# Optimization experiments

Measured on AMD Instinct MI355X. Metric: run time of the kernel, lower is better.

Reference implementation:

```python
import jax, jax.numpy as jnp
import numpy as np

THETA = 1.0
V_TH = 1.0       # spikingjelly IFNode default v_threshold
SG_ALPHA = 4.0   # spikingjelly surrogate.Sigmoid default alpha


@jax.custom_vjp
def heaviside(x):
    # spike = 1 if membrane - threshold >= 0
    return (x >= 0).astype(x.dtype)

def _heaviside_fwd(x):
    return (x >= 0).astype(x.dtype), x

def _heaviside_bwd(x, g):
    s = jax.nn.sigmoid(SG_ALPHA * x)
    return (g * SG_ALPHA * s * (1.0 - s),)

heaviside.defvjp(_heaviside_fwd, _heaviside_bwd)


@jax.custom_vjp
def spike_aggregate(spike_out, z_total):
    return spike_out

def _sa_fwd(spike_out, z_total):
    return spike_out, z_total

def _sa_bwd(z_total, g):
    surrogate = (z_total > 0).astype(g.dtype) / THETA
    return (jnp.zeros_like(g), g * surrogate)

spike_aggregate.defvjp(_sa_fwd, _sa_bwd)


def setup_inputs() -> dict:
    key = jax.random.key(0)
    k_x, k_w1, k_b1, k_w2, k_b2 = jax.random.split(key, 5)
    B, D_in, H, D_out = 4096, 784, 800, 10
    x = jax.random.uniform(k_x, (B, D_in), dtype=jnp.float32)
    # nn.Linear-style init: U(-1/sqrt(fan_in), 1/sqrt(fan_in))
    s1 = 1.0 / np.sqrt(D_in)
    s2 = 1.0 / np.sqrt(H)
    W1 = jax.random.uniform(k_w1, (H, D_in), jnp.float32, -s1, s1)
    b1 = jax.random.uniform(k_b1, (H,), jnp.float32, -s1, s1)
    W2 = jax.random.uniform(k_w2, (D_out, H), jnp.float32, -s2, s2)
    b2 = jax.random.uniform(k_b2, (D_out,), jnp.float32, -s2, s2)
    return {"x": x, "W1": W1, "b1": b1, "W2": W2, "b2": b2, "T_sim": 32}


def reference(x, W1, b1, W2, b2, T_sim):
    B = x.shape[0]
    x = x.reshape(B, -1)
    # fixed Bernoulli rate encoding (rand_like(x) < x)
    u = jax.random.uniform(jax.random.key(42), x.shape, dtype=x.dtype)
    x_fixed = (u < x).astype(x.dtype)
    # fc1 input is the same every timestep -> compute once
    cur1 = x_fixed @ W1.T + b1                     # [B, 800]

    def step(carry, _):
        v1, v2, count, z_total = carry
        h1 = v1 + cur1
        spk1 = heaviside(h1 - V_TH)
        v1 = h1 * (1.0 - jax.lax.stop_gradient(spk1))  # hard reset to 0, detach_reset
        cur2 = spk1 @ W2.T + b2                    # [B, 10]
        z_total = z_total + cur2
        h2 = v2 + cur2
        spk2 = heaviside(h2 - V_TH)
        v2 = h2 * (1.0 - jax.lax.stop_gradient(spk2))
        count = count + spk2
        return (v1, v2, count, z_total), None

    H, D_out = W1.shape[0], W2.shape[0]
    init = (jnp.zeros((B, H), x.dtype), jnp.zeros((B, D_out), x.dtype),
            jnp.zeros((B, D_out), x.dtype), jnp.zeros((B, D_out), x.dtype))
    (v1, v2, count, z_total), _ = jax.lax.scan(step, init, None, length=T_sim)
    return spike_aggregate(count, z_total)
```

## Files before the change

### kernel.cpp

```cpp
#include <hip/hip_runtime.h>
#include <stdint.h>

#define B_ROWS 4096
#define D_IN   784
#define H_DIM  800
#define D_OUT  10
#define T_SIM  32
#define N_ELEM (B_ROWS * D_IN)
#define CAP    448

__device__ __forceinline__ void threefry2x32(uint32_t k0, uint32_t k1,
                                             uint32_t& x0, uint32_t& x1) {
  uint32_t ks0 = k0, ks1 = k1, ks2 = k0 ^ k1 ^ 0x1BD11BDAu;
  x0 += ks0; x1 += ks1;
#define TF_RND(r) { x0 += x1; x1 = (x1 << (r)) | (x1 >> (32 - (r))); x1 ^= x0; }
  TF_RND(13) TF_RND(15) TF_RND(26) TF_RND(6)
  x0 += ks1; x1 += ks2 + 1u;
  TF_RND(17) TF_RND(29) TF_RND(16) TF_RND(24)
  x0 += ks2; x1 += ks0 + 2u;
  TF_RND(13) TF_RND(15) TF_RND(26) TF_RND(6)
  x0 += ks0; x1 += ks1 + 3u;
  TF_RND(17) TF_RND(29) TF_RND(16) TF_RND(24)
  x0 += ks1; x1 += ks2 + 4u;
  TF_RND(13) TF_RND(15) TF_RND(26) TF_RND(6)
  x0 += ks2; x1 += ks0 + 5u;
#undef TF_RND
}

__global__ __launch_bounds__(256) void gen_xfixed(const float* __restrict__ x,
                                                  float* __restrict__ xf) {
  int i = blockIdx.x * blockDim.x + threadIdx.x;
  if (i >= N_ELEM) return;
  uint32_t c0 = 0u, c1 = (uint32_t)i;
  threefry2x32(0u, 42u, c0, c1);
  uint32_t bits = c0 ^ c1;
  float u = __uint_as_float((bits >> 9) | 0x3F800000u) - 1.0f;
  xf[i] = (u < x[i]) ? 1.0f : 0.0f;
}

#define BM 128
#define BN 64
#define BK 16

__global__ __launch_bounds__(256) void gemm_masks(const float* __restrict__ xf,
                                                  const float* __restrict__ W1,
                                                  const float* __restrict__ b1,
                                                  uint32_t* __restrict__ mb) {
  __shared__ __align__(16) float As[BK][BM + 4];
  __shared__ __align__(16) float Bs[BK][BN + 4];
  const int m0 = blockIdx.y * BM;
  const int n0 = blockIdx.x * BN;
  const int t  = threadIdx.x;
  const int tx = t & 15;
  const int ty = t >> 4;
  const int sM = t >> 2;
  const int sK = (t & 3) * 4;
  const int hB = n0 + sM;
  const bool bOK = (hB < H_DIM);
  const float* aptr0 = xf + (size_t)(m0 + sM) * D_IN + sK;
  const float* aptr1 = xf + (size_t)(m0 + 64 + sM) * D_IN + sK;
  const float* bptr  = W1 + (size_t)(bOK ? hB : 0) * D_IN + sK;

  float4 a4a = *(const float4*)(aptr0);
  float4 a4b = *(const float4*)(aptr1);
  float4 b4  = *(const float4*)(bptr);
  if (!bOK) { b4.x = b4.y = b4.z = b4.w = 0.0f; }

  float acc[8][4] = {};
  for (int kt = 0; kt < D_IN; kt += BK) {
    As[sK + 0][sM] = a4a.x; As[sK + 1][sM] = a4a.y;
    As[sK + 2][sM] = a4a.z; As[sK + 3][sM] = a4a.w;
    As[sK + 0][64 + sM] = a4b.x; As[sK + 1][64 + sM] = a4b.y;
    As[sK + 2][64 + sM] = a4b.z; As[sK + 3][64 + sM] = a4b.w;
    Bs[sK + 0][sM] = b4.x; Bs[sK + 1][sM] = b4.y;
    Bs[sK + 2][sM] = b4.z; Bs[sK + 3][sM] = b4.w;
    __syncthreads();
    if (kt + BK < D_IN) {
      a4a = *(const float4*)(aptr0 + kt + BK);
      a4b = *(const float4*)(aptr1 + kt + BK);
      b4  = *(const float4*)(bptr + kt + BK);
      if (!bOK) { b4.x = b4.y = b4.z = b4.w = 0.0f; }
    }
#pragma unroll
    for (int kk = 0; kk < BK; kk++) {
      float4 av0 = *(const float4*)&As[kk][ty * 8];
      float4 av1 = *(const float4*)&As[kk][ty * 8 + 4];
      float4 bv  = *(const float4*)&Bs[kk][tx * 4];
      float a[8] = {av0.x, av0.y, av0.z, av0.w, av1.x, av1.y, av1.z, av1.w};
      float b[4] = {bv.x, bv.y, bv.z, bv.w};
#pragma unroll
      for (int mi = 0; mi < 8; mi++)
#pragma unroll
        for (int ni = 0; ni < 4; ni++)
          acc[mi][ni] = __builtin_fmaf(a[mi], b[ni], acc[mi][ni]);
    }
    __syncthreads();
  }
  const int hOut = n0 + tx * 4;
  if (hOut < H_DIM) {
    float4 bb = *(const float4*)&b1[hOut];
#pragma unroll
    for (int mi = 0; mi < 8; mi++) {
      int m = m0 + ty * 8 + mi;
      float c4[4] = {acc[mi][0] + bb.x, acc[mi][1] + bb.y,
                     acc[mi][2] + bb.z, acc[mi][3] + bb.w};
      uint32_t mk4[4];
#pragma unroll
      for (int ni = 0; ni < 4; ni++) {
        float c = c4[ni];
        float v = 0.0f;
        int p = 0;
#pragma unroll 1
        for (int s = 1; s <= T_SIM; s++) {
          float h1 = v + c;
          if (h1 >= 1.0f) { p = s; break; }
          v = h1;
        }
        uint32_t mk = 0;
        if (p) for (int s = p; s <= T_SIM; s += p) mk |= 1u << (s - 1);
        mk4[ni] = mk;
      }
      *(uint4*)&mb[(size_t)m * H_DIM + hOut] =
          make_uint4(mk4[0], mk4[1], mk4[2], mk4[3]);
    }
  }
}

__global__ __launch_bounds__(320) void snn_scan(const uint32_t* __restrict__ mb,
                                                const float* __restrict__ W2,
                                                const float* __restrict__ b2,
                                                float* __restrict__ out) {
  __shared__ __align__(16) float W2T[H_DIM * D_OUT];
  __shared__ __align__(16) uint2 pkS[2][CAP];
  __shared__ int   lenS[2];
  __shared__ float b2f[D_OUT];
  float* c2s = (float*)&pkS[0][0];
  const int tid  = threadIdx.x;
  const int row0 = blockIdx.x * 2;

  if (tid < D_OUT) b2f[tid] = b2[tid];

  if (tid < 128) {
    const int r = tid >> 6, ln = tid & 63;
    const uint64_t lm = (1ull << ln) - 1ull;
    const uint32_t* mrow = mb + (size_t)(row0 + r) * H_DIM;
    uint32_t mv[13];
#pragma unroll
    for (int ch = 0; ch < 13; ++ch) {
      int h = ch * 64 + ln;
      mv[ch] = (h < H_DIM) ? mrow[h] : 0u;
    }
    int off = 0;
#pragma unroll
    for (int ch = 0; ch < 13; ++ch) {
      bool g = (mv[ch] != 0u);
      uint64_t bal = __ballot(g);
      int pos = off + __popcll(bal & lm);
      if (g && pos < CAP) {
        uint2 pk; pk.x = (uint32_t)((ch * 64 + ln) * 40); pk.y = mv[ch];
        pkS[r][pos] = pk;
      }
      off += __popcll(bal);
    }
    if (off <= CAP) {
      int lp = (off + 63) & ~63;
      int i = off + ln;
      if (i < lp) { pkS[r][i].x = 0u; pkS[r][i].y = 0u; }
    }
    if (ln == 0) lenS[r] = off;
  } else {
    for (int e = tid - 128; e < H_DIM * D_OUT; e += 192) {
      int o = e / H_DIM, h = e - o * H_DIM;
      W2T[h * D_OUT + o] = W2[e];
    }
  }
  __syncthreads();

  float s0 = 0.0f, s1 = 0.0f;
  const int j = tid >> 6;
  const int lane = tid & 63;
  const int t = lane & 31;
  const int r = lane >> 5;
  const bool ovf = (lenS[0] > CAP) || (lenS[1] > CAP);
  {
    if (!ovf) {
      const int Lpad = (lenS[r] + 63) & ~63;
      const uint2* pp = pkS[r];
      const char* wbase = (const char*)W2T + 8 * j;
#pragma unroll 4
      for (int i = 0; i < Lpad; ++i) {
        uint2 pk = pp[i];
        float2 w = *(const float2*)(wbase + pk.x);
        bool g = (pk.y >> t) & 1u;
        s0 += g ? w.x : 0.0f;
        s1 += g ? w.y : 0.0f;
      }
    } else {
      const uint32_t* mrow = mb + (size_t)(row0 + r) * H_DIM;
      const uint32_t vbit = 1u << t;
      for (int h = 0; h < H_DIM; ++h) {
        uint32_t mk = mrow[h];
        float2 w = *(const float2*)&W2T[h * D_OUT + 2 * j];
        s0 += (mk & vbit) ? w.x : 0.0f;
        s1 += (mk & vbit) ? w.y : 0.0f;
      }
    }
  }
  __syncthreads();
  c2s[((r * T_SIM) + t) * D_OUT + 2 * j]     = s0;
  c2s[((r * T_SIM) + t) * D_OUT + 2 * j + 1] = s1;
  __syncthreads();

  if (tid < 2 * D_OUT) {
    const int rr = tid / D_OUT, o = tid % D_OUT;
    const float bb = b2f[o];
    float v = 0.0f; int cnt = 0;
#pragma unroll
    for (int tt = 0; tt < T_SIM; ++tt) {
      float cur2 = c2s[((rr * T_SIM) + tt) * D_OUT + o] + bb;
      float h2 = v + cur2;
      bool spk = (h2 >= 1.0f);
      cnt += spk ? 1 : 0;
      v = spk ? 0.0f : h2;
    }
    out[(size_t)(row0 + rr) * D_OUT + o] = (float)cnt;
  }
}

extern "C" void kernel_launch(void* const* d_in, const int* in_sizes, int n_in,
                              void* d_out, int out_size, void* d_ws, size_t ws_size,
                              hipStream_t stream) {
  const float* x  = (const float*)d_in[0];
  const float* W1 = (const float*)d_in[1];
  const float* b1 = (const float*)d_in[2];
  const float* W2 = (const float*)d_in[3];
  const float* b2 = (const float*)d_in[4];
  float* outp = (float*)d_out;

  float*    xf = (float*)d_ws;
  uint32_t* mbuf = (uint32_t*)(xf + N_ELEM);

  gen_xfixed<<<N_ELEM / 256, 256, 0, stream>>>(x, xf);

  dim3 g1((H_DIM + BN - 1) / BN, B_ROWS / BM);
  gemm_masks<<<g1, 256, 0, stream>>>(xf, W1, b1, mbuf);

  snn_scan<<<B_ROWS / 2, 320, 0, stream>>>(mbuf, W2, b2, outp);
}
```

Before: 317.7 us.

## Replace shared-memory tiled GEMM with register-only single-wave GEMM

```diff
diff --git a/kernel.cpp b/kernel.cpp
--- a/kernel.cpp
+++ b/kernel.cpp
@@ -38,91 +38,97 @@
   xf[i] = (u < x[i]) ? 1.0f : 0.0f;
 }
 
-#define BM 128
-#define BN 64
-#define BK 16
-
-__global__ __launch_bounds__(256) void gemm_masks(const float* __restrict__ xf,
-                                                  const float* __restrict__ W1,
-                                                  const float* __restrict__ b1,
-                                                  uint32_t* __restrict__ mb) {
-  __shared__ __align__(16) float As[BK][BM + 4];
-  __shared__ __align__(16) float Bs[BK][BN + 4];
-  const int m0 = blockIdx.y * BM;
-  const int n0 = blockIdx.x * BN;
-  const int t  = threadIdx.x;
-  const int tx = t & 15;
-  const int ty = t >> 4;
-  const int sM = t >> 2;
-  const int sK = (t & 3) * 4;
-  const int hB = n0 + sM;
-  const bool bOK = (hB < H_DIM);
-  const float* aptr0 = xf + (size_t)(m0 + sM) * D_IN + sK;
-  const float* aptr1 = xf + (size_t)(m0 + 64 + sM) * D_IN + sK;
-  const float* bptr  = W1 + (size_t)(bOK ? hB : 0) * D_IN + sK;
-
-  float4 a4a = *(const float4*)(aptr0);
-  float4 a4b = *(const float4*)(aptr1);
-  float4 b4  = *(const float4*)(bptr);
-  if (!bOK) { b4.x = b4.y = b4.z = b4.w = 0.0f; }
+__global__ __launch_bounds__(64, 3) void gemm_masks(const float* __restrict__ xf,
+                                                    const float* __restrict__ W1,
+                                                    const float* __restrict__ b1,
+                                                    uint32_t* __restrict__ mb) {
+  const int lane = threadIdx.x;
+  const int mq = lane >> 3;
+  const int hq = lane & 7;
+  const int m0 = blockIdx.y * 64 + mq * 8;
+  const int h0 = blockIdx.x * 32 + hq * 4;
+
+  const float* pa[8];
+  const float* pw[4];
+#pragma unroll
+  for (int i = 0; i < 8; i++) pa[i] = xf + (size_t)(m0 + i) * D_IN;
+#pragma unroll
+  for (int j = 0; j < 4; j++) pw[j] = W1 + (size_t)(h0 + j) * D_IN;
 
   float acc[8][4] = {};
-  for (int kt = 0; kt < D_IN; kt += BK) {
-    As[sK + 0][sM] = a4a.x; As[sK + 1][sM] = a4a.y;
-    As[sK + 2][sM] = a4a.z; As[sK + 3][sM] = a4a.w;
-    As[sK + 0][64 + sM] = a4b.x; As[sK + 1][64 + sM] = a4b.y;
-    As[sK + 2][64 + sM] = a4b.z; As[sK + 3][64 + sM] = a4b.w;
-    Bs[sK + 0][sM] = b4.x; Bs[sK + 1][sM] = b4.y;
-    Bs[sK + 2][sM] = b4.z; Bs[sK + 3][sM] = b4.w;
-    __syncthreads();
-    if (kt + BK < D_IN) {
-      a4a = *(const float4*)(aptr0 + kt + BK);
-      a4b = *(const float4*)(aptr1 + kt + BK);
-      b4  = *(const float4*)(bptr + kt + BK);
-      if (!bOK) { b4.x = b4.y = b4.z = b4.w = 0.0f; }
-    }
-#pragma unroll
-    for (int kk = 0; kk < BK; kk++) {
-      float4 av0 = *(const float4*)&As[kk][ty * 8];
-      float4 av1 = *(const float4*)&As[kk][ty * 8 + 4];
-      float4 bv  = *(const float4*)&Bs[kk][tx * 4];
-      float a[8] = {av0.x, av0.y, av0.z, av0.w, av1.x, av1.y, av1.z, av1.w};
-      float b[4] = {bv.x, bv.y, bv.z, bv.w};
-#pragma unroll
-      for (int mi = 0; mi < 8; mi++)
-#pragma unroll
-        for (int ni = 0; ni < 4; ni++)
-          acc[mi][ni] = __builtin_fmaf(a[mi], b[ni], acc[mi][ni]);
-    }
-    __syncthreads();
-  }
-  const int hOut = n0 + tx * 4;
-  if (hOut < H_DIM) {
-    float4 bb = *(const float4*)&b1[hOut];
-#pragma unroll
-    for (int mi = 0; mi < 8; mi++) {
-      int m = m0 + ty * 8 + mi;
-      float c4[4] = {acc[mi][0] + bb.x, acc[mi][1] + bb.y,
-                     acc[mi][2] + bb.z, acc[mi][3] + bb.w};
-      uint32_t mk4[4];
-#pragma unroll
-      for (int ni = 0; ni < 4; ni++) {
-        float c = c4[ni];
-        float v = 0.0f;
-        int p = 0;
+
+  float4 A0[8], B0[4], A1[8], B1[4];
+
+#define LOADS(Ab, Bb, kofs)                                         \
+  {                                                                 \
+    _Pragma("unroll")                                               \
+    for (int i = 0; i < 8; i++)                                     \
+      Ab[i] = *(const float4*)(pa[i] + (kofs));                     \
+    _Pragma("unroll")                                               \
+    for (int j = 0; j < 4; j++)                                     \
+      Bb[j] = *(const float4*)(pw[j] + (kofs));                     \
+  }
+
+#define FMA4(Ab, Bb)                                                \
+  {                                                                 \
+    float a[8], b[4];                                               \
+    _Pragma("unroll")                                               \
+    for (int kk = 0; kk < 4; kk++) {                                \
+      a[0] = ((kk==0)?Ab[0].x:(kk==1)?Ab[0].y:(kk==2)?Ab[0].z:Ab[0].w); \
+      a[1] = ((kk==0)?Ab[1].x:(kk==1)?Ab[1].y:(kk==2)?Ab[1].z:Ab[1].w); \
+      a[2] = ((kk==0)?Ab[2].x:(kk==1)?Ab[2].y:(kk==2)?Ab[2].z:Ab[2].w); \
+      a[3] = ((kk==0)?Ab[3].x:(kk==1)?Ab[3].y:(kk==2)?Ab[3].z:Ab[3].w); \
+      a[4] = ((kk==0)?Ab[4].x:(kk==1)?Ab[4].y:(kk==2)?Ab[4].z:Ab[4].w); \
+      a[5] = ((kk==0)?Ab[5].x:(kk==1)?Ab[5].y:(kk==2)?Ab[5].z:Ab[5].w); \
+      a[6] = ((kk==0)?Ab[6].x:(kk==1)?Ab[6].y:(kk==2)?Ab[6].z:Ab[6].w); \
+      a[7] = ((kk==0)?Ab[7].x:(kk==1)?Ab[7].y:(kk==2)?Ab[7].z:Ab[7].w); \
+      b[0] = ((kk==0)?Bb[0].x:(kk==1)?Bb[0].y:(kk==2)?Bb[0].z:Bb[0].w); \
+      b[1] = ((kk==0)?Bb[1].x:(kk==1)?Bb[1].y:(kk==2)?Bb[1].z:Bb[1].w); \
+      b[2] = ((kk==0)?Bb[2].x:(kk==1)?Bb[2].y:(kk==2)?Bb[2].z:Bb[2].w); \
+      b[3] = ((kk==0)?Bb[3].x:(kk==1)?Bb[3].y:(kk==2)?Bb[3].z:Bb[3].w); \
+      _Pragma("unroll")                                             \
+      for (int mi = 0; mi < 8; mi++)                                \
+        _Pragma("unroll")                                           \
+        for (int hi = 0; hi < 4; hi++)                              \
+          acc[mi][hi] = __builtin_fmaf(a[mi], b[hi], acc[mi][hi]);  \
+    }                                                               \
+  }
+
+  LOADS(A0, B0, 0);
 #pragma unroll 1
-        for (int s = 1; s <= T_SIM; s++) {
-          float h1 = v + c;
-          if (h1 >= 1.0f) { p = s; break; }
-          v = h1;
-        }
-        uint32_t mk = 0;
-        if (p) for (int s = p; s <= T_SIM; s += p) mk |= 1u << (s - 1);
-        mk4[ni] = mk;
-      }
-      *(uint4*)&mb[(size_t)m * H_DIM + hOut] =
-          make_uint4(mk4[0], mk4[1], mk4[2], mk4[3]);
-    }
+  for (int k = 0; k < D_IN; k += 8) {
+    LOADS(A1, B1, k + 4);
+    FMA4(A0, B0);
+    if (k + 8 < D_IN) LOADS(A0, B0, k + 8);
+    FMA4(A1, B1);
+  }
+#undef LOADS
+#undef FMA4
+
+  float4 bb = *(const float4*)&b1[h0];
+#pragma unroll
+  for (int mi = 0; mi < 8; mi++) {
+    int m = m0 + mi;
+    float c4[4] = {acc[mi][0] + bb.x, acc[mi][1] + bb.y,
+                   acc[mi][2] + bb.z, acc[mi][3] + bb.w};
+    uint32_t mk4[4];
+#pragma unroll
+    for (int ni = 0; ni < 4; ni++) {
+      float c = c4[ni];
+      float v = 0.0f;
+      int p = 0;
+#pragma unroll 1
+      for (int s = 1; s <= T_SIM; s++) {
+        float h1 = v + c;
+        if (h1 >= 1.0f) { p = s; break; }
+        v = h1;
+      }
+      uint32_t mk = 0;
+      if (p) for (int s = p; s <= T_SIM; s += p) mk |= 1u << (s - 1);
+      mk4[ni] = mk;
+    }
+    *(uint4*)&mb[(size_t)m * H_DIM + h0] =
+        make_uint4(mk4[0], mk4[1], mk4[2], mk4[3]);
   }
 }
 
@@ -242,8 +248,8 @@
 
   gen_xfixed<<<N_ELEM / 256, 256, 0, stream>>>(x, xf);
 
-  dim3 g1((H_DIM + BN - 1) / BN, B_ROWS / BM);
-  gemm_masks<<<g1, 256, 0, stream>>>(xf, W1, b1, mbuf);
+  dim3 g1(H_DIM / 32, B_ROWS / 64);
+  gemm_masks<<<g1, 64, 0, stream>>>(xf, W1, b1, mbuf);
 
   snn_scan<<<B_ROWS / 2, 320, 0, stream>>>(mbuf, W2, b2, outp);
 }
```

After: 594.2 us. 87.1% more time.

## Halve GEMM row tile and double-buffer shared memory tiles

Applied to the files above, without the earlier changes.

```diff
diff --git a/kernel.cpp b/kernel.cpp
--- a/kernel.cpp
+++ b/kernel.cpp
@@ -38,7 +38,7 @@
   xf[i] = (u < x[i]) ? 1.0f : 0.0f;
 }
 
-#define BM 128
+#define BM 64
 #define BN 64
 #define BK 16
 
@@ -46,62 +46,70 @@
                                                   const float* __restrict__ W1,
                                                   const float* __restrict__ b1,
                                                   uint32_t* __restrict__ mb) {
-  __shared__ __align__(16) float As[BK][BM + 4];
-  __shared__ __align__(16) float Bs[BK][BN + 4];
+  __shared__ __align__(16) float As[2][BK][BM + 4];
+  __shared__ __align__(16) float Bs[2][BK][BN + 4];
   const int m0 = blockIdx.y * BM;
   const int n0 = blockIdx.x * BN;
   const int t  = threadIdx.x;
-  const int tx = t & 15;
-  const int ty = t >> 4;
+  const int tx = t & 15, ty = t >> 4;
   const int sM = t >> 2;
   const int sK = (t & 3) * 4;
   const int hB = n0 + sM;
   const bool bOK = (hB < H_DIM);
-  const float* aptr0 = xf + (size_t)(m0 + sM) * D_IN + sK;
-  const float* aptr1 = xf + (size_t)(m0 + 64 + sM) * D_IN + sK;
-  const float* bptr  = W1 + (size_t)(bOK ? hB : 0) * D_IN + sK;
-
-  float4 a4a = *(const float4*)(aptr0);
-  float4 a4b = *(const float4*)(aptr1);
-  float4 b4  = *(const float4*)(bptr);
+  const float* aptr = xf + (size_t)(m0 + sM) * D_IN + sK;
+  const float* bptr = W1 + (size_t)(bOK ? hB : 0) * D_IN + sK;
+
+  float4 a4 = *(const float4*)(aptr);
+  float4 b4 = *(const float4*)(bptr);
   if (!bOK) { b4.x = b4.y = b4.z = b4.w = 0.0f; }
 
-  float acc[8][4] = {};
-  for (int kt = 0; kt < D_IN; kt += BK) {
-    As[sK + 0][sM] = a4a.x; As[sK + 1][sM] = a4a.y;
-    As[sK + 2][sM] = a4a.z; As[sK + 3][sM] = a4a.w;
-    As[sK + 0][64 + sM] = a4b.x; As[sK + 1][64 + sM] = a4b.y;
-    As[sK + 2][64 + sM] = a4b.z; As[sK + 3][64 + sM] = a4b.w;
-    Bs[sK + 0][sM] = b4.x; Bs[sK + 1][sM] = b4.y;
-    Bs[sK + 2][sM] = b4.z; Bs[sK + 3][sM] = b4.w;
-    __syncthreads();
-    if (kt + BK < D_IN) {
-      a4a = *(const float4*)(aptr0 + kt + BK);
-      a4b = *(const float4*)(aptr1 + kt + BK);
-      b4  = *(const float4*)(bptr + kt + BK);
+  As[0][sK + 0][sM] = a4.x; As[0][sK + 1][sM] = a4.y;
+  As[0][sK + 2][sM] = a4.z; As[0][sK + 3][sM] = a4.w;
+  Bs[0][sK + 0][sM] = b4.x; Bs[0][sK + 1][sM] = b4.y;
+  Bs[0][sK + 2][sM] = b4.z; Bs[0][sK + 3][sM] = b4.w;
+  __syncthreads();
+
+  float acc[4][4] = {};
+  const int NT = D_IN / BK;
+#pragma unroll 1
+  for (int tt = 0; tt < NT; ++tt) {
+    const int cur = tt & 1;
+    const bool more = (tt + 1 < NT);
+    if (more) {
+      a4 = *(const float4*)(aptr + (tt + 1) * BK);
+      b4 = *(const float4*)(bptr + (tt + 1) * BK);
       if (!bOK) { b4.x = b4.y = b4.z = b4.w = 0.0f; }
     }
+    const float (*Ac)[BM + 4] = As[cur];
+    const float (*Bc)[BN + 4] = Bs[cur];
 #pragma unroll
     for (int kk = 0; kk < BK; kk++) {
-      float4 av0 = *(const float4*)&As[kk][ty * 8];
-      float4 av1 = *(const float4*)&As[kk][ty * 8 + 4];
-      float4 bv  = *(const float4*)&Bs[kk][tx * 4];
-      float a[8] = {av0.x, av0.y, av0.z, av0.w, av1.x, av1.y, av1.z, av1.w};
+      float4 av = *(const float4*)&Ac[kk][ty * 4];
+      float4 bv = *(const float4*)&Bc[kk][tx * 4];
+      float a[4] = {av.x, av.y, av.z, av.w};
       float b[4] = {bv.x, bv.y, bv.z, bv.w};
 #pragma unroll
-      for (int mi = 0; mi < 8; mi++)
+      for (int mi = 0; mi < 4; mi++)
 #pragma unroll
         for (int ni = 0; ni < 4; ni++)
           acc[mi][ni] = __builtin_fmaf(a[mi], b[ni], acc[mi][ni]);
     }
-    __syncthreads();
-  }
+    if (more) {
+      const int nxt = cur ^ 1;
+      As[nxt][sK + 0][sM] = a4.x; As[nxt][sK + 1][sM] = a4.y;
+      As[nxt][sK + 2][sM] = a4.z; As[nxt][sK + 3][sM] = a4.w;
+      Bs[nxt][sK + 0][sM] = b4.x; Bs[nxt][sK + 1][sM] = b4.y;
+      Bs[nxt][sK + 2][sM] = b4.z; Bs[nxt][sK + 3][sM] = b4.w;
+      __syncthreads();
+    }
+  }
+
   const int hOut = n0 + tx * 4;
   if (hOut < H_DIM) {
     float4 bb = *(const float4*)&b1[hOut];
 #pragma unroll
-    for (int mi = 0; mi < 8; mi++) {
-      int m = m0 + ty * 8 + mi;
+    for (int mi = 0; mi < 4; mi++) {
+      int m = m0 + ty * 4 + mi;
       float c4[4] = {acc[mi][0] + bb.x, acc[mi][1] + bb.y,
                      acc[mi][2] + bb.z, acc[mi][3] + bb.w};
       uint32_t mk4[4];
```

After: 304.4 us. 4.2% less time.
